# Kernel optimization log

Measured on AMD Instinct MI355X. Metric: run time of the kernel, lower is better.

Reference implementation:

```python
import jax, jax.numpy as jnp
import numpy as np

N = 50000
E = 800000
IN_DIM = 256
HID = 32
HEADS = 4
OUT_DIM = 40
NEG_SLOPE = 0.2


def gat_layer(x, src, dst, W, a_src, a_dst, b, n_nodes, heads, ch, concat):
    # x: [N, F_in], W: [F_in, heads*ch], a_src/a_dst: [heads, ch], b: [out]
    h = (x @ W).reshape(n_nodes, heads, ch)                 # [N,H,C]
    alpha_s = jnp.einsum('nhc,hc->nh', h, a_src)            # [N,H]
    alpha_d = jnp.einsum('nhc,hc->nh', h, a_dst)            # [N,H]
    e = jax.nn.leaky_relu(alpha_s[src] + alpha_d[dst], NEG_SLOPE)  # [E,H]
    # segment softmax over destination neighborhoods (self-loops guarantee nonempty)
    m = jax.ops.segment_max(e, dst, num_segments=n_nodes)   # [N,H]
    e = jnp.exp(e - m[dst])
    denom = jax.ops.segment_sum(e, dst, num_segments=n_nodes)
    alpha = e / (denom[dst] + 1e-16)                         # [E,H]
    msg = h[src] * alpha[:, :, None]                         # [E,H,C]
    out = jax.ops.segment_sum(msg, dst, num_segments=n_nodes)  # [N,H,C]
    out = out.reshape(n_nodes, heads * ch) if concat else out.mean(axis=1)
    return out + b


def setup_inputs() -> dict:
    key = jax.random.key(0)
    ks = jax.random.split(key, 10)
    x = jax.random.normal(ks[0], (N, IN_DIM), dtype=jnp.float32)
    edge_index = jax.random.randint(ks[1], (2, E), 0, N, dtype=jnp.int32)
    s1 = 1.0 / np.sqrt(IN_DIM)
    s2 = 1.0 / np.sqrt(HID * HEADS)
    return {
        'x': x,
        'edge_index': edge_index,
        'W1': jax.random.normal(ks[2], (IN_DIM, HEADS * HID), dtype=jnp.float32) * s1,
        'a_src1': jax.random.normal(ks[3], (HEADS, HID), dtype=jnp.float32) * s1,
        'a_dst1': jax.random.normal(ks[4], (HEADS, HID), dtype=jnp.float32) * s1,
        'b1': jnp.zeros((HEADS * HID,), dtype=jnp.float32),
        'W2': jax.random.normal(ks[5], (HEADS * HID, OUT_DIM), dtype=jnp.float32) * s2,
        'a_src2': jax.random.normal(ks[6], (1, OUT_DIM), dtype=jnp.float32) * s2,
        'a_dst2': jax.random.normal(ks[7], (1, OUT_DIM), dtype=jnp.float32) * s2,
        'b2': jnp.zeros((OUT_DIM,), dtype=jnp.float32),
    }


def reference(x, edge_index, W1, a_src1, a_dst1, b1, W2, a_src2, a_dst2, b2):
    # PyG GATConv adds self-loops by default
    loops = jnp.arange(N, dtype=edge_index.dtype)
    src = jnp.concatenate([edge_index[0], loops])
    dst = jnp.concatenate([edge_index[1], loops])
    h = gat_layer(x, src, dst, W1, a_src1, a_dst1, b1, N, HEADS, HID, True)
    h = jax.nn.relu(h)
    out = gat_layer(h, src, dst, W2, a_src2, a_dst2, b2, N, 1, OUT_DIM, False)
    return jax.nn.log_softmax(out, axis=1)
```

## Files before the change

### kernel.cpp

```cpp
#include <hip/hip_runtime.h>
#include <math.h>

#define N_NODES 50000
#define N_EDGES 800000
#define IN_DIM  256
#define F1      128
#define HEADS   4
#define OUT_DIM 40
#define NEG     0.2f

#define NB   391
#define CAP  3072
#define EB   4096

#define DCAP 96

typedef __attribute__((ext_vector_type(8))) short short8;
typedef __attribute__((ext_vector_type(4))) float float4v;

__device__ __forceinline__ unsigned short f2bf(float f) {
  unsigned int u = __float_as_uint(f);
  u += 0x7FFF + ((u >> 16) & 1);
  return (unsigned short)(u >> 16);
}
__device__ __forceinline__ float bf2f(unsigned short h) {
  return __uint_as_float((unsigned int)h << 16);
}
__device__ __forceinline__ float bflo(unsigned int u) { return __uint_as_float(u << 16); }
__device__ __forceinline__ float bfhi(unsigned int u) { return __uint_as_float(u & 0xffff0000u); }

__device__ __forceinline__ float lrelu(float e) { return e > 0.f ? e : e * NEG; }

__global__ __launch_bounds__(256) void bin_kernel(const int* __restrict__ ei,
                                                  int* __restrict__ gcnt,
                                                  int2* __restrict__ gbucket) {
  __shared__ int ls[EB];
  __shared__ int ld[EB];
  __shared__ int lcnt[NB];
  __shared__ int lcur[NB];
  __shared__ int gbaseS[NB];
  int tid = threadIdx.x;
  size_t base = (size_t)blockIdx.x * EB;
  for (int t = tid; t < NB; t += 256) { lcnt[t] = 0; lcur[t] = 0; }
  __syncthreads();
#pragma unroll
  for (int l = 0; l < EB / 256; l++) {
    int li = l * 256 + tid;
    size_t idx = base + li;
    int s = 0, d = -1;
    if (idx < N_EDGES) {
      s = ei[idx];
      d = ei[N_EDGES + idx];
      atomicAdd(&lcnt[d >> 7], 1);
    }
    ls[li] = s;
    ld[li] = d;
  }
  __syncthreads();
  for (int t = tid; t < NB; t += 256) gbaseS[t] = atomicAdd(&gcnt[t], lcnt[t]);
  __syncthreads();
#pragma unroll
  for (int l = 0; l < EB / 256; l++) {
    int li = l * 256 + tid;
    int d = ld[li];
    if (d >= 0) {
      int b = d >> 7;
      int r = gbaseS[b] + atomicAdd(&lcur[b], 1);
      if (r >= CAP) r = CAP - 1;
      gbucket[(size_t)b * CAP + r] = make_int2(ls[li], d);
    }
  }
}

__global__ __launch_bounds__(512) void bucketscan_kernel(const int* __restrict__ gcnt,
                                                         int* __restrict__ bbase,
                                                         int* __restrict__ row_ptr) {
  __shared__ int lds[512];
  int tid = threadIdx.x;
  int v = (tid < NB) ? gcnt[tid] : 0;
  lds[tid] = v;
  __syncthreads();
  for (int off = 1; off < 512; off <<= 1) {
    int t = (tid >= off) ? lds[tid - off] : 0;
    __syncthreads();
    lds[tid] += t;
    __syncthreads();
  }
  if (tid < NB) bbase[tid] = lds[tid] - v;
  if (tid == 0) row_ptr[N_NODES] = N_EDGES;
}

__global__ __launch_bounds__(256) void csr_kernel(const int2* __restrict__ gbucket,
                                                  const int* __restrict__ gcnt,
                                                  const int* __restrict__ bbase,
                                                  int* __restrict__ row_ptr,
                                                  int* __restrict__ col) {
  __shared__ int2 ent[CAP];
  __shared__ int hcnt[128];
  __shared__ int sc[128];
  __shared__ int cur[128];
  int b = blockIdx.x;
  int tid = threadIdx.x;
  int cnt = gcnt[b]; if (cnt > CAP) cnt = CAP;
  int base = bbase[b];
  if (tid < 128) hcnt[tid] = 0;
  __syncthreads();
  for (int i = tid; i < cnt; i += 256) {
    int2 e = gbucket[(size_t)b * CAP + i];
    ent[i] = e;
    atomicAdd(&hcnt[e.y & 127], 1);
  }
  __syncthreads();
  if (tid < 128) sc[tid] = hcnt[tid];
  __syncthreads();
  for (int off = 1; off < 128; off <<= 1) {
    int t = 0;
    if (tid < 128 && tid >= off) t = sc[tid - off];
    __syncthreads();
    if (tid < 128) sc[tid] += t;
    __syncthreads();
  }
  if (tid < 128) {
    int excl = sc[tid] - hcnt[tid];
    cur[tid] = excl;
    int node = (b << 7) + tid;
    if (node < N_NODES) row_ptr[node] = base + excl;
  }
  __syncthreads();
  for (int i = tid; i < cnt; i += 256) {
    int2 e = ent[i];
    int r = atomicAdd(&cur[e.y & 127], 1);
    col[base + r] = e.x;
  }
}

__global__ __launch_bounds__(256) void w1pack_kernel(const float* __restrict__ W1,
                                                     unsigned short* __restrict__ wHi,
                                                     unsigned short* __restrict__ wLo) {
  int tid = blockIdx.x * 256 + threadIdx.x;
  int kk = tid >> 9;
  int rest = tid & 511;
  int t = rest >> 6;
  int lane = rest & 63;
  int q = lane >> 4;
  int ln = lane & 15;
  int n = t * 16 + ln;
  unsigned int hi[4], lo[4];
#pragma unroll
  for (int jj = 0; jj < 4; jj++) {
    unsigned short h0, h1, l0, l1;
    {
      float v = W1[(kk * 32 + q * 8 + jj * 2) * F1 + n];
      h0 = f2bf(v); l0 = f2bf(v - bf2f(h0));
    }
    {
      float v = W1[(kk * 32 + q * 8 + jj * 2 + 1) * F1 + n];
      h1 = f2bf(v); l1 = f2bf(v - bf2f(h1));
    }
    hi[jj] = (unsigned int)h0 | ((unsigned int)h1 << 16);
    lo[jj] = (unsigned int)l0 | ((unsigned int)l1 << 16);
  }
  size_t base = (size_t)tid * 8;
  *(uint4*)&wHi[base] = make_uint4(hi[0], hi[1], hi[2], hi[3]);
  *(uint4*)&wLo[base] = make_uint4(lo[0], lo[1], lo[2], lo[3]);
}

__global__ __launch_bounds__(256) void gemm1_mfma_kernel(
    const float* __restrict__ x, const unsigned short* __restrict__ wHi,
    const unsigned short* __restrict__ wLo,
    const float* __restrict__ a_src, const float* __restrict__ a_dst,
    unsigned short* __restrict__ h1b, float* __restrict__ as1, float* __restrict__ ad1) {
  int tid = threadIdx.x;
  int w = tid >> 6;
  int lane = tid & 63;
  int q = lane >> 4;
  int ln = lane & 15;
  int rowBase = blockIdx.x * 64 + w * 16;
  int rowA = rowBase + ln;
  int rowAc = rowA < N_NODES ? rowA : N_NODES - 1;
  float4v acc[8];
#pragma unroll
  for (int t = 0; t < 8; t++) acc[t] = (float4v){0.f, 0.f, 0.f, 0.f};
  const short8* bhp = (const short8*)wHi;
  const short8* blp = (const short8*)wLo;
  for (int kk = 0; kk < 8; kk++) {
    const float4* xp = (const float4*)(x + (size_t)rowAc * IN_DIM + kk * 32 + q * 8);
    float4 a0 = xp[0];
    float4 a1 = xp[1];
    float av[8] = {a0.x, a0.y, a0.z, a0.w, a1.x, a1.y, a1.z, a1.w};
    short8 ahi, alo;
#pragma unroll
    for (int j = 0; j < 8; j++) {
      unsigned short h = f2bf(av[j]);
      ahi[j] = (short)h;
      alo[j] = (short)f2bf(av[j] - bf2f(h));
    }
    int fbase = (kk * 8) * 64 + lane;
#pragma unroll
    for (int t = 0; t < 8; t++) {
      short8 bh = bhp[fbase + t * 64];
      short8 bl = blp[fbase + t * 64];
      acc[t] = __builtin_amdgcn_mfma_f32_16x16x32_bf16(ahi, bh, acc[t], 0, 0, 0);
      acc[t] = __builtin_amdgcn_mfma_f32_16x16x32_bf16(ahi, bl, acc[t], 0, 0, 0);
      acc[t] = __builtin_amdgcn_mfma_f32_16x16x32_bf16(alo, bh, acc[t], 0, 0, 0);
    }
  }
  float asv[8], adv[8];
#pragma unroll
  for (int t = 0; t < 8; t++) {
    asv[t] = a_src[t * 16 + ln];
    adv[t] = a_dst[t * 16 + ln];
  }
#pragma unroll
  for (int reg = 0; reg < 4; reg++) {
    int r = rowBase + q * 4 + reg;
    bool valid = (r < N_NODES);
    if (valid) {
#pragma unroll
      for (int t = 0; t < 8; t++)
        h1b[(size_t)r * F1 + t * 16 + ln] = f2bf(acc[t][reg]);
    }
#pragma unroll
    for (int h = 0; h < 4; h++) {
      float sa = acc[2 * h][reg] * asv[2 * h] + acc[2 * h + 1][reg] * asv[2 * h + 1];
      float sd = acc[2 * h][reg] * adv[2 * h] + acc[2 * h + 1][reg] * adv[2 * h + 1];
#pragma unroll
      for (int off = 1; off < 16; off <<= 1) {
        sa += __shfl_xor(sa, off);
        sd += __shfl_xor(sd, off);
      }
      if (ln == 0 && valid) {
        as1[r * 4 + h] = sa;
        ad1[r * 4 + h] = sd;
      }
    }
  }
}

__global__ __launch_bounds__(256) void gather1_kernel(
    const unsigned short* __restrict__ h1b, const float* __restrict__ as1,
    const float* __restrict__ ad1, const float* __restrict__ b1,
    const int* __restrict__ row_ptr, const int* __restrict__ col,
    float* __restrict__ x2) {
  __shared__ float4 wsh[4][DCAP];
  __shared__ int ssh[4][DCAP];
  int wv = threadIdx.x >> 6;
  int n = blockIdx.x * 4 + wv;
  if (n >= N_NODES) return;
  int lane = threadIdx.x & 63;
  int start = row_ptr[n];
  int deg = row_ptr[n + 1] - start;
  bool fast = (deg + 1) <= DCAP;
  float4 ad = *(const float4*)&ad1[n * 4];
  float s0 = 0.f, s1 = 0.f, s2 = 0.f, s3 = 0.f;
  for (int i = lane; i <= deg; i += 64) {
    int src = (i < deg) ? col[start + i] : n;
    float4 as = *(const float4*)&as1[src * 4];
    float e0 = __expf(lrelu(as.x + ad.x));
    float e1 = __expf(lrelu(as.y + ad.y));
    float e2 = __expf(lrelu(as.z + ad.z));
    float e3 = __expf(lrelu(as.w + ad.w));
    s0 += e0; s1 += e1; s2 += e2; s3 += e3;
    if (fast) {
      ssh[wv][i] = src;
      wsh[wv][i] = make_float4(e0, e1, e2, e3);
    }
  }
#pragma unroll
  for (int off = 32; off > 0; off >>= 1) {
    s0 += __shfl_xor(s0, off);
    s1 += __shfl_xor(s1, off);
    s2 += __shfl_xor(s2, off);
    s3 += __shfl_xor(s3, off);
  }
  int slot = lane >> 4;
  int lane16 = lane & 15;
  int head = lane16 >> 2;
  float rsh = (head == 0) ? s0 : (head == 1) ? s1 : (head == 2) ? s2 : s3;
  rsh = 1.f / (rsh + 1e-16f);
  float4 accA = make_float4(0.f, 0.f, 0.f, 0.f);
  float4 accB = make_float4(0.f, 0.f, 0.f, 0.f);
  if (fast) {
    const float* wp = (const float*)&wsh[wv][0];
    int i = slot;
    for (; i + 4 <= deg; i += 8) {
      int sA = ssh[wv][i];
      int sB = ssh[wv][i + 4];
      float wA = wp[i * 4 + head] * rsh;
      float wB = wp[(i + 4) * 4 + head] * rsh;
      uint4 uA = *(const uint4*)(h1b + (size_t)sA * F1 + lane16 * 8);
      uint4 uB = *(const uint4*)(h1b + (size_t)sB * F1 + lane16 * 8);
      accA.x += wA * bflo(uA.x); accA.y += wA * bfhi(uA.x);
      accA.z += wA * bflo(uA.y); accA.w += wA * bfhi(uA.y);
      accB.x += wA * bflo(uA.z); accB.y += wA * bfhi(uA.z);
      accB.z += wA * bflo(uA.w); accB.w += wA * bfhi(uA.w);
      accA.x += wB * bflo(uB.x); accA.y += wB * bfhi(uB.x);
      accA.z += wB * bflo(uB.y); accA.w += wB * bfhi(uB.y);
      accB.x += wB * bflo(uB.z); accB.y += wB * bfhi(uB.z);
      accB.z += wB * bflo(uB.w); accB.w += wB * bfhi(uB.w);
    }
    if (i <= deg) {
      int s = ssh[wv][i];
      float w = wp[i * 4 + head] * rsh;
      uint4 u = *(const uint4*)(h1b + (size_t)s * F1 + lane16 * 8);
      accA.x += w * bflo(u.x); accA.y += w * bfhi(u.x);
      accA.z += w * bflo(u.y); accA.w += w * bfhi(u.y);
      accB.x += w * bflo(u.z); accB.y += w * bfhi(u.z);
      accB.z += w * bflo(u.w); accB.w += w * bfhi(u.w);
    }
  } else {
    float adh = (head == 0) ? ad.x : (head == 1) ? ad.y : (head == 2) ? ad.z : ad.w;
    for (int i = slot; i <= deg; i += 4) {
      int src = (i < deg) ? col[start + i] : n;
      float w = __expf(lrelu(as1[src * 4 + head] + adh)) * rsh;
      uint4 u = *(const uint4*)(h1b + (size_t)src * F1 + lane16 * 8);
      accA.x += w * bflo(u.x); accA.y += w * bfhi(u.x);
      accA.z += w * bflo(u.y); accA.w += w * bfhi(u.y);
      accB.x += w * bflo(u.z); accB.y += w * bfhi(u.z);
      accB.z += w * bflo(u.w); accB.w += w * bfhi(u.w);
    }
  }
#pragma unroll
  for (int off = 16; off <= 32; off <<= 1) {
    accA.x += __shfl_xor(accA.x, off); accA.y += __shfl_xor(accA.y, off);
    accA.z += __shfl_xor(accA.z, off); accA.w += __shfl_xor(accA.w, off);
    accB.x += __shfl_xor(accB.x, off); accB.y += __shfl_xor(accB.y, off);
    accB.z += __shfl_xor(accB.z, off); accB.w += __shfl_xor(accB.w, off);
  }
  if (slot == 0) {
    float4 bA = *(const float4*)&b1[lane16 * 8];
    float4 bB = *(const float4*)&b1[lane16 * 8 + 4];
    float4 oA, oB;
    oA.x = fmaxf(accA.x + bA.x, 0.f); oA.y = fmaxf(accA.y + bA.y, 0.f);
    oA.z = fmaxf(accA.z + bA.z, 0.f); oA.w = fmaxf(accA.w + bA.w, 0.f);
    oB.x = fmaxf(accB.x + bB.x, 0.f); oB.y = fmaxf(accB.y + bB.y, 0.f);
    oB.z = fmaxf(accB.z + bB.z, 0.f); oB.w = fmaxf(accB.w + bB.w, 0.f);
    *(float4*)&x2[(size_t)n * F1 + lane16 * 8] = oA;
    *(float4*)&x2[(size_t)n * F1 + lane16 * 8 + 4] = oB;
  }
}

__global__ __launch_bounds__(256) void gemm2_kernel(
    const float* __restrict__ x2, const float* __restrict__ W2,
    const float* __restrict__ asv, const float* __restrict__ adv,
    unsigned short* __restrict__ h2b, float* __restrict__ as2, float* __restrict__ ad2) {
  __shared__ float xs[64][132];
  __shared__ float W2s[128][44];
  __shared__ float asv_s[40], adv_s[40];
  int tid = threadIdx.x;
  int bm = blockIdx.x * 64;
#pragma unroll
  for (int l = 0; l < 8; l++) {
    int idx = tid + l * 256;
    int r = idx >> 5;
    int c4 = (idx & 31) << 2;
    float4 v = make_float4(0.f, 0.f, 0.f, 0.f);
    if (bm + r < N_NODES) v = *(const float4*)&x2[(size_t)(bm + r) * F1 + c4];
    *(float4*)&xs[r][c4] = v;
  }
#pragma unroll
  for (int l = 0; l < 5; l++) {
    int idx = tid + l * 256;
    int k = idx / 10;
    int c4 = (idx - k * 10) * 4;
    *(float4*)&W2s[k][c4] = *(const float4*)&W2[k * OUT_DIM + c4];
  }
  if (tid < OUT_DIM) { asv_s[tid] = asv[tid]; adv_s[tid] = adv[tid]; }
  __syncthreads();
  int r = tid >> 2;
  int cb = (tid & 3) * 10;
  float acc[10] = {0.f};
  for (int k = 0; k < F1; k++) {
    float xv = xs[r][k];
#pragma unroll
    for (int c = 0; c < 10; c++) acc[c] += xv * W2s[k][cb + c];
  }
  int grow = bm + r;
  float sa = 0.f, sd = 0.f;
#pragma unroll
  for (int c = 0; c < 10; c++) {
    sa += acc[c] * asv_s[cb + c];
    sd += acc[c] * adv_s[cb + c];
  }
#pragma unroll
  for (int off = 1; off < 4; off <<= 1) {
    sa += __shfl_xor(sa, off);
    sd += __shfl_xor(sd, off);
  }
  if (grow < N_NODES) {
#pragma unroll
    for (int c = 0; c < 10; c += 2) {
      unsigned int p = ((unsigned int)f2bf(acc[c + 1]) << 16) | f2bf(acc[c]);
      *(unsigned int*)&h2b[(size_t)grow * OUT_DIM + cb + c] = p;
    }
    if ((tid & 3) == 0) { as2[grow] = sa; ad2[grow] = sd; }
  }
}

__global__ __launch_bounds__(256) void gather2_kernel(
    const unsigned short* __restrict__ h2b, const float* __restrict__ as2,
    const float* __restrict__ ad2, const float* __restrict__ b2,
    const int* __restrict__ row_ptr, const int* __restrict__ col,
    float* __restrict__ out) {
  __shared__ float w2sh[4][DCAP];
  __shared__ int s2sh[4][DCAP];
  int wv = threadIdx.x >> 6;
  int n = blockIdx.x * 4 + wv;
  if (n >= N_NODES) return;
  int lane = threadIdx.x & 63;
  int start = row_ptr[n];
  int deg = row_ptr[n + 1] - start;
  bool fast = (deg + 1) <= DCAP;
  float adh = ad2[n];
  float part = 0.f;
  for (int i = lane; i <= deg; i += 64) {
    int src = (i < deg) ? col[start + i] : n;
    float e = __expf(lrelu(as2[src] + adh));
    part += e;
    if (fast) { s2sh[wv][i] = src; w2sh[wv][i] = e; }
  }
#pragma unroll
  for (int off = 32; off > 0; off >>= 1) part += __shfl_xor(part, off);
  float rs = 1.f / (part + 1e-16f);
  int slot = lane / 5;
  int c = lane - slot * 5;
  float4 accA = make_float4(0.f, 0.f, 0.f, 0.f);
  float4 accB = make_float4(0.f, 0.f, 0.f, 0.f);
  if (slot < 12) {
    if (fast) {
      for (int i = slot; i <= deg; i += 12) {
        int src = s2sh[wv][i];
        float wgt = w2sh[wv][i] * rs;
        uint4 u = *(const uint4*)(h2b + (size_t)src * OUT_DIM + c * 8);
        accA.x += wgt * bflo(u.x); accA.y += wgt * bfhi(u.x);
        accA.z += wgt * bflo(u.y); accA.w += wgt * bfhi(u.y);
        accB.x += wgt * bflo(u.z); accB.y += wgt * bfhi(u.z);
        accB.z += wgt * bflo(u.w); accB.w += wgt * bfhi(u.w);
      }
    } else {
      for (int i = slot; i <= deg; i += 12) {
        int src = (i < deg) ? col[start + i] : n;
        float wgt = __expf(lrelu(as2[src] + adh)) * rs;
        uint4 u = *(const uint4*)(h2b + (size_t)src * OUT_DIM + c * 8);
        accA.x += wgt * bflo(u.x); accA.y += wgt * bfhi(u.x);
        accA.z += wgt * bflo(u.y); accA.w += wgt * bfhi(u.y);
        accB.x += wgt * bflo(u.z); accB.y += wgt * bfhi(u.z);
        accB.z += wgt * bflo(u.w); accB.w += wgt * bfhi(u.w);
      }
    }
  }
  {
    float v[8] = {accA.x, accA.y, accA.z, accA.w, accB.x, accB.y, accB.z, accB.w};
#pragma unroll
    for (int k = 0; k < 8; k++) v[k] += __shfl(v[k], lane + 30);
#pragma unroll
    for (int k = 0; k < 8; k++) v[k] += __shfl(v[k], lane + 15);
    float t1[8], t2[8];
#pragma unroll
    for (int k = 0; k < 8; k++) t1[k] = __shfl(v[k], lane + 5);
#pragma unroll
    for (int k = 0; k < 8; k++) t2[k] = __shfl(v[k], lane + 10);
#pragma unroll
    for (int k = 0; k < 8; k++) v[k] += t1[k] + t2[k];
    accA.x = v[0]; accA.y = v[1]; accA.z = v[2]; accA.w = v[3];
    accB.x = v[4]; accB.y = v[5]; accB.z = v[6]; accB.w = v[7];
  }
  bool owner = (slot == 0);
  float vals[8] = {accA.x, accA.y, accA.z, accA.w, accB.x, accB.y, accB.z, accB.w};
  float lmax = -1e30f, lsum = 0.f;
  if (owner) {
#pragma unroll
    for (int k = 0; k < 8; k++) {
      vals[k] += b2[c * 8 + k];
      lmax = fmaxf(lmax, vals[k]);
    }
  }
  float gmax = lmax;
#pragma unroll
  for (int off = 32; off > 0; off >>= 1) gmax = fmaxf(gmax, __shfl_xor(gmax, off));
  if (owner) {
#pragma unroll
    for (int k = 0; k < 8; k++) lsum += __expf(vals[k] - gmax);
  }
#pragma unroll
  for (int off = 32; off > 0; off >>= 1) lsum += __shfl_xor(lsum, off);
  if (owner) {
    float lse = gmax + __logf(lsum);
    float4 oA = make_float4(vals[0] - lse, vals[1] - lse, vals[2] - lse, vals[3] - lse);
    float4 oB = make_float4(vals[4] - lse, vals[5] - lse, vals[6] - lse, vals[7] - lse);
    *(float4*)&out[(size_t)n * OUT_DIM + c * 8] = oA;
    *(float4*)&out[(size_t)n * OUT_DIM + c * 8 + 4] = oB;
  }
}

extern "C" void kernel_launch(void* const* d_in, const int* in_sizes, int n_in,
                              void* d_out, int out_size, void* d_ws, size_t ws_size,
                              hipStream_t stream) {
  const float* x      = (const float*)d_in[0];
  const int*   ei     = (const int*)d_in[1];
  const float* W1     = (const float*)d_in[2];
  const float* a_src1 = (const float*)d_in[3];
  const float* a_dst1 = (const float*)d_in[4];
  const float* b1     = (const float*)d_in[5];
  const float* W2     = (const float*)d_in[6];
  const float* a_src2 = (const float*)d_in[7];
  const float* a_dst2 = (const float*)d_in[8];
  const float* b2     = (const float*)d_in[9];
  float* out = (float*)d_out;

  char* ws = (char*)d_ws;
  size_t off = 0;
  auto alloc = [&](size_t bytes) -> void* {
    void* p = ws + off;
    off += (bytes + 255) & ~(size_t)255;
    return p;
  };
  unsigned short* h1b = (unsigned short*)alloc((size_t)N_NODES * F1 * 2);
  unsigned short* h2b = (unsigned short*)alloc((size_t)N_NODES * OUT_DIM * 2);
  unsigned short* wHi = (unsigned short*)alloc((size_t)IN_DIM * F1 * 2);
  unsigned short* wLo = (unsigned short*)alloc((size_t)IN_DIM * F1 * 2);
  float* as1    = (float*)alloc((size_t)N_NODES * HEADS * 4);
  float* ad1    = (float*)alloc((size_t)N_NODES * HEADS * 4);
  float* x2     = (float*)alloc((size_t)N_NODES * F1 * 4);
  float* as2    = (float*)alloc((size_t)N_NODES * 4);
  float* ad2    = (float*)alloc((size_t)N_NODES * 4);
  int* row_ptr  = (int*)alloc((size_t)(N_NODES + 1) * 4);
  int* col      = (int*)alloc((size_t)N_EDGES * 4);
  int* gcnt     = (int*)alloc((size_t)NB * 4);
  int* bbase    = (int*)alloc((size_t)NB * 4);
  int2* gbucket = (int2*)alloc((size_t)NB * CAP * 8);

  hipMemsetAsync(gcnt, 0, (size_t)NB * 4, stream);
  bin_kernel<<<(N_EDGES + EB - 1) / EB, 256, 0, stream>>>(ei, gcnt, gbucket);
  bucketscan_kernel<<<1, 512, 0, stream>>>(gcnt, bbase, row_ptr);
  csr_kernel<<<NB, 256, 0, stream>>>(gbucket, gcnt, bbase, row_ptr, col);

  w1pack_kernel<<<16, 256, 0, stream>>>(W1, wHi, wLo);
  gemm1_mfma_kernel<<<(N_NODES + 63) / 64, 256, 0, stream>>>(
      x, wHi, wLo, a_src1, a_dst1, h1b, as1, ad1);
  gather1_kernel<<<(N_NODES + 3) / 4, 256, 0, stream>>>(h1b, as1, ad1, b1, row_ptr, col, x2);

  gemm2_kernel<<<(N_NODES + 63) / 64, 256, 0, stream>>>(x2, W2, a_src2, a_dst2, h2b, as2, ad2);
  gather2_kernel<<<(N_NODES + 3) / 4, 256, 0, stream>>>(h2b, as2, ad2, b2, row_ptr, col, out);
}
```

Measured before the change: 257.2 us.

## Split GEMM1 output columns across two blocks and unroll gather1 4-way

The first-layer MFMA GEMM now launches twice as many blocks, each computing half of the 128 output features (two of the four heads), which halves accumulator registers per wave and raises occupancy and parallelism. The cost is that each x row is loaded and split into hi/lo bf16 twice. Separately, the fast path of the gather1 edge loop is unrolled from 2 to 4 neighbors per iteration to put more independent loads in flight, with a strided remainder loop replacing the single tail step.

```diff
diff --git a/kernel.cpp b/kernel.cpp
--- a/kernel.cpp
+++ b/kernel.cpp
@@ -175,12 +175,15 @@
   int lane = tid & 63;
   int q = lane >> 4;
   int ln = lane & 15;
-  int rowBase = blockIdx.x * 64 + w * 16;
+  int b = blockIdx.x;
+  int rowBlk = b >> 1;
+  int half = b & 1;
+  int rowBase = rowBlk * 64 + w * 16;
   int rowA = rowBase + ln;
   int rowAc = rowA < N_NODES ? rowA : N_NODES - 1;
-  float4v acc[8];
-#pragma unroll
-  for (int t = 0; t < 8; t++) acc[t] = (float4v){0.f, 0.f, 0.f, 0.f};
+  float4v acc[4];
+#pragma unroll
+  for (int t = 0; t < 4; t++) acc[t] = (float4v){0.f, 0.f, 0.f, 0.f};
   const short8* bhp = (const short8*)wHi;
   const short8* blp = (const short8*)wLo;
   for (int kk = 0; kk < 8; kk++) {
@@ -195,9 +198,9 @@
       ahi[j] = (short)h;
       alo[j] = (short)f2bf(av[j] - bf2f(h));
     }
-    int fbase = (kk * 8) * 64 + lane;
-#pragma unroll
-    for (int t = 0; t < 8; t++) {
+    int fbase = (kk * 8 + half * 4) * 64 + lane;
+#pragma unroll
+    for (int t = 0; t < 4; t++) {
       short8 bh = bhp[fbase + t * 64];
       short8 bl = blp[fbase + t * 64];
       acc[t] = __builtin_amdgcn_mfma_f32_16x16x32_bf16(ahi, bh, acc[t], 0, 0, 0);
@@ -205,11 +208,11 @@
       acc[t] = __builtin_amdgcn_mfma_f32_16x16x32_bf16(alo, bh, acc[t], 0, 0, 0);
     }
   }
-  float asv[8], adv[8];
-#pragma unroll
-  for (int t = 0; t < 8; t++) {
-    asv[t] = a_src[t * 16 + ln];
-    adv[t] = a_dst[t * 16 + ln];
+  float asv[4], adv[4];
+#pragma unroll
+  for (int t = 0; t < 4; t++) {
+    asv[t] = a_src[half * 64 + t * 16 + ln];
+    adv[t] = a_dst[half * 64 + t * 16 + ln];
   }
 #pragma unroll
   for (int reg = 0; reg < 4; reg++) {
@@ -217,21 +220,21 @@
     bool valid = (r < N_NODES);
     if (valid) {
 #pragma unroll
-      for (int t = 0; t < 8; t++)
-        h1b[(size_t)r * F1 + t * 16 + ln] = f2bf(acc[t][reg]);
-    }
-#pragma unroll
-    for (int h = 0; h < 4; h++) {
-      float sa = acc[2 * h][reg] * asv[2 * h] + acc[2 * h + 1][reg] * asv[2 * h + 1];
-      float sd = acc[2 * h][reg] * adv[2 * h] + acc[2 * h + 1][reg] * adv[2 * h + 1];
+      for (int t = 0; t < 4; t++)
+        h1b[(size_t)r * F1 + half * 64 + t * 16 + ln] = f2bf(acc[t][reg]);
+    }
+#pragma unroll
+    for (int lh = 0; lh < 2; lh++) {
+      float sa = acc[2 * lh][reg] * asv[2 * lh] + acc[2 * lh + 1][reg] * asv[2 * lh + 1];
+      float sd = acc[2 * lh][reg] * adv[2 * lh] + acc[2 * lh + 1][reg] * adv[2 * lh + 1];
 #pragma unroll
       for (int off = 1; off < 16; off <<= 1) {
         sa += __shfl_xor(sa, off);
         sd += __shfl_xor(sd, off);
       }
       if (ln == 0 && valid) {
-        as1[r * 4 + h] = sa;
-        ad1[r * 4 + h] = sd;
+        as1[r * 4 + half * 2 + lh] = sa;
+        ad1[r * 4 + half * 2 + lh] = sd;
       }
     }
   }
@@ -283,13 +286,19 @@
   if (fast) {
     const float* wp = (const float*)&wsh[wv][0];
     int i = slot;
-    for (; i + 4 <= deg; i += 8) {
+    for (; i + 12 <= deg; i += 16) {
       int sA = ssh[wv][i];
       int sB = ssh[wv][i + 4];
+      int sC = ssh[wv][i + 8];
+      int sD = ssh[wv][i + 12];
       float wA = wp[i * 4 + head] * rsh;
       float wB = wp[(i + 4) * 4 + head] * rsh;
+      float wC = wp[(i + 8) * 4 + head] * rsh;
+      float wD = wp[(i + 12) * 4 + head] * rsh;
       uint4 uA = *(const uint4*)(h1b + (size_t)sA * F1 + lane16 * 8);
       uint4 uB = *(const uint4*)(h1b + (size_t)sB * F1 + lane16 * 8);
+      uint4 uC = *(const uint4*)(h1b + (size_t)sC * F1 + lane16 * 8);
+      uint4 uD = *(const uint4*)(h1b + (size_t)sD * F1 + lane16 * 8);
       accA.x += wA * bflo(uA.x); accA.y += wA * bfhi(uA.x);
       accA.z += wA * bflo(uA.y); accA.w += wA * bfhi(uA.y);
       accB.x += wA * bflo(uA.z); accB.y += wA * bfhi(uA.z);
@@ -298,8 +307,16 @@
       accA.z += wB * bflo(uB.y); accA.w += wB * bfhi(uB.y);
       accB.x += wB * bflo(uB.z); accB.y += wB * bfhi(uB.z);
       accB.z += wB * bflo(uB.w); accB.w += wB * bfhi(uB.w);
-    }
-    if (i <= deg) {
+      accA.x += wC * bflo(uC.x); accA.y += wC * bfhi(uC.x);
+      accA.z += wC * bflo(uC.y); accA.w += wC * bfhi(uC.y);
+      accB.x += wC * bflo(uC.z); accB.y += wC * bfhi(uC.z);
+      accB.z += wC * bflo(uC.w); accB.w += wC * bfhi(uC.w);
+      accA.x += wD * bflo(uD.x); accA.y += wD * bfhi(uD.x);
+      accA.z += wD * bflo(uD.y); accA.w += wD * bfhi(uD.y);
+      accB.x += wD * bflo(uD.z); accB.y += wD * bfhi(uD.z);
+      accB.z += wD * bflo(uD.w); accB.w += wD * bfhi(uD.w);
+    }
+    for (; i <= deg; i += 4) {
       int s = ssh[wv][i];
       float w = wp[i * 4 + head] * rsh;
       uint4 u = *(const uint4*)(h1b + (size_t)s * F1 + lane16 * 8);
@@ -536,7 +553,7 @@
   csr_kernel<<<NB, 256, 0, stream>>>(gbucket, gcnt, bbase, row_ptr, col);
 
   w1pack_kernel<<<16, 256, 0, stream>>>(W1, wHi, wLo);
-  gemm1_mfma_kernel<<<(N_NODES + 63) / 64, 256, 0, stream>>>(
+  gemm1_mfma_kernel<<<2 * ((N_NODES + 63) / 64), 256, 0, stream>>>(
       x, wHi, wLo, a_src1, a_dst1, h1b, as1, ad1);
   gather1_kernel<<<(N_NODES + 3) / 4, 256, 0, stream>>>(h1b, as1, ad1, b1, row_ptr, col, x2);
 
```

New measurement: 263.1 us. +2.3%, slower.
